# Kernel tuning notes

Hardware: AMD Instinct MI355X
Metric: run time of the kernel (lower is better)

Reference implementation:

```python
import jax, jax.numpy as jnp
import numpy as np

IN_CH = 128
EMBED = 64
ALPHA = 0.2  # leaky relu slope
NEG_INF = jnp.float32(-9e15)


def setup_inputs() -> dict:
    key = jax.random.key(0)
    k_x, k_adj, k_W, k_a, k_b = jax.random.split(key, 5)
    B, N = 2, 512
    x = jax.random.normal(k_x, (B, N, IN_CH), dtype=jnp.float32)
    adj = jax.random.randint(k_adj, (B, N, N), 0, 2, dtype=jnp.int32)
    # xavier_uniform with gain=1.414
    gain = 1.414
    lim_W = gain * np.sqrt(6.0 / (IN_CH + EMBED))
    W = jax.random.uniform(k_W, (IN_CH, EMBED), jnp.float32, -lim_W, lim_W)
    lim_a = gain * np.sqrt(6.0 / (2 * EMBED + 1))
    a = jax.random.uniform(k_a, (2 * EMBED, 1), jnp.float32, -lim_a, lim_a)
    bias = jax.random.normal(k_b, (EMBED,), dtype=jnp.float32) * 0.02
    return {"x": x, "adj": adj, "W": W, "a": a, "bias": bias}


def reference(x, adj, W, a, bias):
    B, N, _ = x.shape
    D = W.shape[1]
    hidden = jnp.matmul(x, W)                      # [B, N, D]
    # Faithful reproduction of the original's repeat_interleave/repeat + cat(dim=1) + view.
    chunks = jnp.repeat(hidden, N, axis=1)         # [B, N*N, D]
    alt = jnp.tile(hidden, (1, N, 1))              # [B, N*N, D]
    allc = jnp.concatenate([chunks, alt], axis=1).reshape(B, N, N, 2 * D)
    attn = jnp.matmul(allc, a)[..., 0]             # [B, N, N]
    attn = jnp.where(attn >= 0, attn, ALPHA * attn)  # leaky relu
    attn = jnp.where(adj > 0, attn, NEG_INF)
    attention = jax.nn.softmax(attn, axis=-1)
    # dropout omitted: reference is eval-mode (deterministic)
    out = jnp.matmul(attention, hidden) + bias     # [B, N, D]
    return out
```

## Files before the change

### kernel.cpp

```cpp
#include <hip/hip_runtime.h>
#include <math.h>

#define GN 512
#define GB 2
#define INCH 128
#define GD 64
#define ALPHA 0.2f
#define NEG_INF_F (-9e15f)
#define TI 4

__global__ __launch_bounds__(256) void k_hidden(
        const float* __restrict__ x, const float* __restrict__ W,
        const float* __restrict__ a,
        float* __restrict__ hidden, float* __restrict__ s1,
        float* __restrict__ s2, float* __restrict__ s12) {
    const int row0 = blockIdx.x * 4;
    const int tid = threadIdx.x;
    __shared__ float Wl[INCH * GD];
    __shared__ float xs[4][INCH];

    const float4* W4 = (const float4*)W;
    float4* Wl4 = (float4*)Wl;
    #pragma unroll
    for (int idx = tid; idx < INCH * GD / 4; idx += 256) Wl4[idx] = W4[idx];
    const float4* x4 = (const float4*)(x + (size_t)row0 * INCH);
    if (tid < 4 * INCH / 4) ((float4*)xs)[tid] = x4[tid];
    __syncthreads();

    const int r = tid >> 6, d = tid & 63;
    float h = 0.f;
    #pragma unroll
    for (int k = 0; k < INCH; ++k) h = fmaf(xs[r][k], Wl[k * GD + d], h);
    hidden[(size_t)(row0 + r) * GD + d] = h;

    float p1 = a[d] * h, p2 = a[GD + d] * h;
    #pragma unroll
    for (int off = 32; off > 0; off >>= 1) {
        p1 += __shfl_xor(p1, off, 64);
        p2 += __shfl_xor(p2, off, 64);
    }
    if (d == 0) { s1[row0 + r] = p1; s2[row0 + r] = p2; s12[row0 + r] = p1 + p2; }
}

__global__ __launch_bounds__(512) void k_attn(
        const int* __restrict__ adj, const float* __restrict__ hidden,
        const float* __restrict__ s1, const float* __restrict__ s2,
        const float* __restrict__ s12, const float* __restrict__ bias,
        float* __restrict__ out) {
    const int blk = blockIdx.x;
    const int b = blk >> 7;
    const int i0 = (blk & 127) * TI;
    const int tid = threadIdx.x;
    const int lane = tid & 63;
    const int w = tid >> 6;

    __shared__ float pl[TI][GN];
    __shared__ float red[8][TI][GD];
    __shared__ float invs[TI];

    const float* s1b  = s1  + b * GN;
    const float* s2b  = s2  + b * GN;
    const float* s12b = s12 + b * GN;

    if (w < TI) {
        const int i = i0 + w;
        const int* adjrow = adj + ((size_t)b * GN + i) * GN;
        float v[8];
        if (i < 256) {
            float c0 = s12b[2 * i], c1 = s12b[2 * i + 1];
            c0 = c0 >= 0.f ? c0 : ALPHA * c0;
            c1 = c1 >= 0.f ? c1 : ALPHA * c1;
            #pragma unroll
            for (int seg = 0; seg < 8; ++seg) {
                const int j = seg * 64 + lane;
                v[seg] = adjrow[j] > 0 ? (seg < 4 ? c0 : c1) : NEG_INF_F;
            }
        } else {
            #pragma unroll
            for (int seg = 0; seg < 8; ++seg) {
                const int j = seg * 64 + lane;
                const int m = j & 255;
                float pre = s1b[2 * m] + s2b[2 * m + 1];
                pre = pre >= 0.f ? pre : ALPHA * pre;
                v[seg] = adjrow[j] > 0 ? pre : NEG_INF_F;
            }
        }
        float mx = v[0];
        #pragma unroll
        for (int seg = 1; seg < 8; ++seg) mx = fmaxf(mx, v[seg]);
        #pragma unroll
        for (int off = 32; off > 0; off >>= 1) mx = fmaxf(mx, __shfl_xor(mx, off, 64));
        float s = 0.f;
        #pragma unroll
        for (int seg = 0; seg < 8; ++seg) {
            const float e = expf(v[seg] - mx);
            pl[w][seg * 64 + lane] = e;
            s += e;
        }
        #pragma unroll
        for (int off = 32; off > 0; off >>= 1) s += __shfl_xor(s, off, 64);
        if (lane == 0) invs[w] = 1.f / s;
    }
    __syncthreads();

    const float* hb = hidden + (size_t)b * GN * GD;
    const int j0 = w * 64;
    float acc0 = 0.f, acc1 = 0.f, acc2 = 0.f, acc3 = 0.f;
    #pragma unroll 4
    for (int jj = 0; jj < 64; jj += 4) {
        const int j = j0 + jj;
        const float4 q0 = *(const float4*)&pl[0][j];
        const float4 q1 = *(const float4*)&pl[1][j];
        const float4 q2 = *(const float4*)&pl[2][j];
        const float4 q3 = *(const float4*)&pl[3][j];
        float hv;
        hv = hb[(size_t)(j + 0) * GD + lane];
        acc0 = fmaf(q0.x, hv, acc0); acc1 = fmaf(q1.x, hv, acc1);
        acc2 = fmaf(q2.x, hv, acc2); acc3 = fmaf(q3.x, hv, acc3);
        hv = hb[(size_t)(j + 1) * GD + lane];
        acc0 = fmaf(q0.y, hv, acc0); acc1 = fmaf(q1.y, hv, acc1);
        acc2 = fmaf(q2.y, hv, acc2); acc3 = fmaf(q3.y, hv, acc3);
        hv = hb[(size_t)(j + 2) * GD + lane];
        acc0 = fmaf(q0.z, hv, acc0); acc1 = fmaf(q1.z, hv, acc1);
        acc2 = fmaf(q2.z, hv, acc2); acc3 = fmaf(q3.z, hv, acc3);
        hv = hb[(size_t)(j + 3) * GD + lane];
        acc0 = fmaf(q0.w, hv, acc0); acc1 = fmaf(q1.w, hv, acc1);
        acc2 = fmaf(q2.w, hv, acc2); acc3 = fmaf(q3.w, hv, acc3);
    }
    red[w][0][lane] = acc0; red[w][1][lane] = acc1;
    red[w][2][lane] = acc2; red[w][3][lane] = acc3;
    __syncthreads();

    if (tid < TI * GD) {
        const int r = tid >> 6, d = tid & 63;
        float o = 0.f;
        #pragma unroll
        for (int ww = 0; ww < 8; ++ww) o += red[ww][r][d];
        o = o * invs[r] + bias[d];
        out[((size_t)b * GN + i0 + r) * GD + d] = o;
    }
}

extern "C" void kernel_launch(void* const* d_in, const int* in_sizes, int n_in,
                              void* d_out, int out_size, void* d_ws, size_t ws_size,
                              hipStream_t stream) {
    const float* x    = (const float*)d_in[0];
    const int*   adj  = (const int*)d_in[1];
    const float* W    = (const float*)d_in[2];
    const float* a    = (const float*)d_in[3];
    const float* bias = (const float*)d_in[4];
    float* out = (float*)d_out;

    float* ws     = (float*)d_ws;
    float* hidden = ws;
    float* s1f    = hidden + GB * GN * GD;
    float* s2f    = s1f + GB * GN;
    float* s12f   = s2f + GB * GN;

    k_hidden<<<GB * GN / 4, 256, 0, stream>>>(x, W, a, hidden, s1f, s2f, s12f);
    k_attn<<<GB * GN / TI, 512, 0, stream>>>(adj, hidden, s1f, s2f, s12f, bias, out);
}
```

Before: 15.92 us.

## Fuse projection and attention into one kernel with per-block bf16 MFMA recompute

Merges the two launches into one kernel. Each block recomputes the full per-batch hidden projection (512x64) using bf16 MFMA with a swizzled shared-memory copy of W, keeps hidden and the attention scores in LDS, and stages its adj rows in LDS. This removes the second launch and the global round trip for hidden and scores. In exchange every block repeats the whole batch projection, about 128x redundant compute, and hidden is now rounded to bf16, which lowers precision. The large LDS footprint limits occupancy.

```diff
diff --git a/kernel.cpp b/kernel.cpp
--- a/kernel.cpp
+++ b/kernel.cpp
@@ -9,80 +9,152 @@
 #define NEG_INF_F (-9e15f)
 #define TI 4
 
-__global__ __launch_bounds__(256) void k_hidden(
-        const float* __restrict__ x, const float* __restrict__ W,
-        const float* __restrict__ a,
-        float* __restrict__ hidden, float* __restrict__ s1,
-        float* __restrict__ s2, float* __restrict__ s12) {
-    const int row0 = blockIdx.x * 4;
-    const int tid = threadIdx.x;
-    __shared__ float Wl[INCH * GD];
-    __shared__ float xs[4][INCH];
-
-    const float4* W4 = (const float4*)W;
-    float4* Wl4 = (float4*)Wl;
-    #pragma unroll
-    for (int idx = tid; idx < INCH * GD / 4; idx += 256) Wl4[idx] = W4[idx];
-    const float4* x4 = (const float4*)(x + (size_t)row0 * INCH);
-    if (tid < 4 * INCH / 4) ((float4*)xs)[tid] = x4[tid];
-    __syncthreads();
-
-    const int r = tid >> 6, d = tid & 63;
-    float h = 0.f;
-    #pragma unroll
-    for (int k = 0; k < INCH; ++k) h = fmaf(xs[r][k], Wl[k * GD + d], h);
-    hidden[(size_t)(row0 + r) * GD + d] = h;
-
-    float p1 = a[d] * h, p2 = a[GD + d] * h;
-    #pragma unroll
-    for (int off = 32; off > 0; off >>= 1) {
-        p1 += __shfl_xor(p1, off, 64);
-        p2 += __shfl_xor(p2, off, 64);
-    }
-    if (d == 0) { s1[row0 + r] = p1; s2[row0 + r] = p2; s12[row0 + r] = p1 + p2; }
-}
-
-__global__ __launch_bounds__(512) void k_attn(
-        const int* __restrict__ adj, const float* __restrict__ hidden,
-        const float* __restrict__ s1, const float* __restrict__ s2,
-        const float* __restrict__ s12, const float* __restrict__ bias,
-        float* __restrict__ out) {
+typedef float f32x4 __attribute__((ext_vector_type(4)));
+typedef short short8 __attribute__((ext_vector_type(8)));
+
+#define HB_OFF  0
+#define ADJ_OFF 65536
+#define S1_OFF  73728
+#define S2_OFF  75776
+#define INV_OFF 77824
+#define UN_OFF  77888
+#define LDS_BYTES 94272
+
+__device__ __forceinline__ unsigned f2bf(float f) {
+    unsigned u = __float_as_uint(f);
+    return (u + 0x7FFFu + ((u >> 16) & 1u)) >> 16;
+}
+__device__ __forceinline__ float bf2f(unsigned short h) {
+    return __uint_as_float(((unsigned)h) << 16);
+}
+
+__global__ __launch_bounds__(512, 2) void k_fused(
+        const float* __restrict__ x, const int* __restrict__ adj,
+        const float* __restrict__ W, const float* __restrict__ a,
+        const float* __restrict__ bias, float* __restrict__ out) {
+    extern __shared__ char smem[];
     const int blk = blockIdx.x;
-    const int b = blk >> 7;
-    const int i0 = (blk & 127) * TI;
     const int tid = threadIdx.x;
     const int lane = tid & 63;
     const int w = tid >> 6;
-
-    __shared__ float pl[TI][GN];
-    __shared__ float red[8][TI][GD];
-    __shared__ float invs[TI];
-
-    const float* s1b  = s1  + b * GN;
-    const float* s2b  = s2  + b * GN;
-    const float* s12b = s12 + b * GN;
+    const int lane15 = lane & 15;
+    const int kg = lane >> 4;
+    const int b = blk >> 7;
+    const int i0 = (blk & 127) * TI;
+
+    short* hbf  = (short*)(smem + HB_OFF);
+    int*   adjl = (int*)(smem + ADJ_OFF);
+    float* s1l  = (float*)(smem + S1_OFF);
+    float* s2l  = (float*)(smem + S2_OFF);
+    float* invs = (float*)(smem + INV_OFF);
+    short* wt   = (short*)(smem + UN_OFF);
+    float* plf  = (float*)(smem + UN_OFF);
+    float* red  = (float*)(smem + UN_OFF + 8192);
+
+    #pragma unroll
+    for (int rep = 0; rep < 4; ++rep) {
+        const int idx = tid + rep * 512;
+        const float4 wv = ((const float4*)W)[idx];
+        const int k = idx >> 4;
+        const int n0 = (idx & 15) * 4;
+        #pragma unroll
+        for (int e = 0; e < 4; ++e) {
+            const int n = n0 + e;
+            const float f = (e == 0) ? wv.x : (e == 1) ? wv.y : (e == 2) ? wv.z : wv.w;
+            wt[n * 128 + (((k >> 3) ^ (n & 7)) << 3) + (k & 7)] = (short)f2bf(f);
+        }
+    }
+    ((int4*)adjl)[tid] = ((const int4*)(adj + ((size_t)b * GN + i0) * GN))[tid];
+    float a1v[4], a2v[4];
+    #pragma unroll
+    for (int ct = 0; ct < 4; ++ct) {
+        a1v[ct] = a[ct * 16 + lane15];
+        a2v[ct] = a[GD + ct * 16 + lane15];
+    }
+    __syncthreads();
+
+    const float* xw = x + ((size_t)b * GN + w * 64) * INCH;
+    f32x4 acc[4][4];
+    #pragma unroll
+    for (int mt = 0; mt < 4; ++mt)
+        #pragma unroll
+        for (int ct = 0; ct < 4; ++ct)
+            acc[mt][ct] = (f32x4)0.f;
+
+    #pragma unroll
+    for (int kt = 0; kt < 4; ++kt) {
+        short8 av[4];
+        #pragma unroll
+        for (int mt = 0; mt < 4; ++mt) {
+            const float* p = xw + (mt * 16 + lane15) * INCH + kt * 32 + kg * 8;
+            const float4 lo = *((const float4*)p);
+            const float4 hi = *((const float4*)(p + 4));
+            int4 ai;
+            ai.x = f2bf(lo.x) | (f2bf(lo.y) << 16);
+            ai.y = f2bf(lo.z) | (f2bf(lo.w) << 16);
+            ai.z = f2bf(hi.x) | (f2bf(hi.y) << 16);
+            ai.w = f2bf(hi.z) | (f2bf(hi.w) << 16);
+            av[mt] = __builtin_bit_cast(short8, ai);
+        }
+        #pragma unroll
+        for (int ct = 0; ct < 4; ++ct) {
+            const int n = ct * 16 + lane15;
+            const int c = kt * 4 + kg;
+            const short8 bv = *((const short8*)(smem + UN_OFF + n * 256 + ((c ^ (n & 7)) << 4)));
+            #pragma unroll
+            for (int mt = 0; mt < 4; ++mt)
+                acc[mt][ct] = __builtin_amdgcn_mfma_f32_16x16x32_bf16(
+                                  av[mt], bv, acc[mt][ct], 0, 0, 0);
+        }
+    }
+
+    #pragma unroll
+    for (int mt = 0; mt < 4; ++mt) {
+        #pragma unroll
+        for (int r = 0; r < 4; ++r) {
+            float t1 = acc[mt][0][r] * a1v[0] + acc[mt][1][r] * a1v[1]
+                     + acc[mt][2][r] * a1v[2] + acc[mt][3][r] * a1v[3];
+            float t2 = acc[mt][0][r] * a2v[0] + acc[mt][1][r] * a2v[1]
+                     + acc[mt][2][r] * a2v[2] + acc[mt][3][r] * a2v[3];
+            #pragma unroll
+            for (int off = 1; off < 16; off <<= 1) {
+                t1 += __shfl_xor(t1, off, 64);
+                t2 += __shfl_xor(t2, off, 64);
+            }
+            const int row = w * 64 + mt * 16 + kg * 4 + r;
+            if (lane15 == 0) { s1l[row] = t1; s2l[row] = t2; }
+        }
+    }
+    #pragma unroll
+    for (int mt = 0; mt < 4; ++mt)
+        #pragma unroll
+        for (int ct = 0; ct < 4; ++ct)
+            #pragma unroll
+            for (int r = 0; r < 4; ++r) {
+                const int row = w * 64 + mt * 16 + kg * 4 + r;
+                hbf[row * GD + ct * 16 + lane15] = (short)f2bf(acc[mt][ct][r]);
+            }
+    __syncthreads();
 
     if (w < TI) {
         const int i = i0 + w;
-        const int* adjrow = adj + ((size_t)b * GN + i) * GN;
+        const int* adjw = adjl + w * GN;
         float v[8];
         if (i < 256) {
-            float c0 = s12b[2 * i], c1 = s12b[2 * i + 1];
+            float c0 = s1l[2 * i] + s2l[2 * i];
+            float c1 = s1l[2 * i + 1] + s2l[2 * i + 1];
             c0 = c0 >= 0.f ? c0 : ALPHA * c0;
             c1 = c1 >= 0.f ? c1 : ALPHA * c1;
             #pragma unroll
+            for (int seg = 0; seg < 8; ++seg)
+                v[seg] = adjw[seg * 64 + lane] > 0 ? (seg < 4 ? c0 : c1) : NEG_INF_F;
+        } else {
+            #pragma unroll
             for (int seg = 0; seg < 8; ++seg) {
-                const int j = seg * 64 + lane;
-                v[seg] = adjrow[j] > 0 ? (seg < 4 ? c0 : c1) : NEG_INF_F;
-            }
-        } else {
-            #pragma unroll
-            for (int seg = 0; seg < 8; ++seg) {
-                const int j = seg * 64 + lane;
-                const int m = j & 255;
-                float pre = s1b[2 * m] + s2b[2 * m + 1];
+                const int m = (seg * 64 + lane) & 255;
+                float pre = s1l[2 * m] + s2l[2 * m + 1];
                 pre = pre >= 0.f ? pre : ALPHA * pre;
-                v[seg] = adjrow[j] > 0 ? pre : NEG_INF_F;
+                v[seg] = adjw[seg * 64 + lane] > 0 ? pre : NEG_INF_F;
             }
         }
         float mx = v[0];
@@ -94,7 +166,7 @@
         #pragma unroll
         for (int seg = 0; seg < 8; ++seg) {
             const float e = expf(v[seg] - mx);
-            pl[w][seg * 64 + lane] = e;
+            plf[(seg * 64 + lane) * 4 + w] = e;
             s += e;
         }
         #pragma unroll
@@ -103,39 +175,27 @@
     }
     __syncthreads();
 
-    const float* hb = hidden + (size_t)b * GN * GD;
     const int j0 = w * 64;
-    float acc0 = 0.f, acc1 = 0.f, acc2 = 0.f, acc3 = 0.f;
+    float o0 = 0.f, o1 = 0.f, o2 = 0.f, o3 = 0.f;
     #pragma unroll 4
-    for (int jj = 0; jj < 64; jj += 4) {
+    for (int jj = 0; jj < 64; ++jj) {
         const int j = j0 + jj;
-        const float4 q0 = *(const float4*)&pl[0][j];
-        const float4 q1 = *(const float4*)&pl[1][j];
-        const float4 q2 = *(const float4*)&pl[2][j];
-        const float4 q3 = *(const float4*)&pl[3][j];
-        float hv;
-        hv = hb[(size_t)(j + 0) * GD + lane];
-        acc0 = fmaf(q0.x, hv, acc0); acc1 = fmaf(q1.x, hv, acc1);
-        acc2 = fmaf(q2.x, hv, acc2); acc3 = fmaf(q3.x, hv, acc3);
-        hv = hb[(size_t)(j + 1) * GD + lane];
-        acc0 = fmaf(q0.y, hv, acc0); acc1 = fmaf(q1.y, hv, acc1);
-        acc2 = fmaf(q2.y, hv, acc2); acc3 = fmaf(q3.y, hv, acc3);
-        hv = hb[(size_t)(j + 2) * GD + lane];
-        acc0 = fmaf(q0.z, hv, acc0); acc1 = fmaf(q1.z, hv, acc1);
-        acc2 = fmaf(q2.z, hv, acc2); acc3 = fmaf(q3.z, hv, acc3);
-        hv = hb[(size_t)(j + 3) * GD + lane];
-        acc0 = fmaf(q0.w, hv, acc0); acc1 = fmaf(q1.w, hv, acc1);
-        acc2 = fmaf(q2.w, hv, acc2); acc3 = fmaf(q3.w, hv, acc3);
-    }
-    red[w][0][lane] = acc0; red[w][1][lane] = acc1;
-    red[w][2][lane] = acc2; red[w][3][lane] = acc3;
+        const float4 q = *((const float4*)(plf + j * 4));
+        const float h = bf2f((unsigned short)hbf[j * GD + lane]);
+        o0 = fmaf(q.x, h, o0); o1 = fmaf(q.y, h, o1);
+        o2 = fmaf(q.z, h, o2); o3 = fmaf(q.w, h, o3);
+    }
+    red[(w * 4 + 0) * 64 + lane] = o0;
+    red[(w * 4 + 1) * 64 + lane] = o1;
+    red[(w * 4 + 2) * 64 + lane] = o2;
+    red[(w * 4 + 3) * 64 + lane] = o3;
     __syncthreads();
 
     if (tid < TI * GD) {
         const int r = tid >> 6, d = tid & 63;
         float o = 0.f;
         #pragma unroll
-        for (int ww = 0; ww < 8; ++ww) o += red[ww][r][d];
+        for (int ww = 0; ww < 8; ++ww) o += red[(ww * 4 + r) * 64 + d];
         o = o * invs[r] + bias[d];
         out[((size_t)b * GN + i0 + r) * GD + d] = o;
     }
@@ -151,12 +211,7 @@
     const float* bias = (const float*)d_in[4];
     float* out = (float*)d_out;
 
-    float* ws     = (float*)d_ws;
-    float* hidden = ws;
-    float* s1f    = hidden + GB * GN * GD;
-    float* s2f    = s1f + GB * GN;
-    float* s12f   = s2f + GB * GN;
-
-    k_hidden<<<GB * GN / 4, 256, 0, stream>>>(x, W, a, hidden, s1f, s2f, s12f);
-    k_attn<<<GB * GN / TI, 512, 0, stream>>>(adj, hidden, s1f, s2f, s12f, bias, out);
-}
+    (void)hipFuncSetAttribute((const void*)k_fused,
+                              hipFuncAttributeMaxDynamicSharedMemorySize, LDS_BYTES);
+    k_fused<<<GB * GN / TI, 512, LDS_BYTES, stream>>>(x, adj, W, a, bias, out);
+}
```

Result: slower. 21.49 us (+34.9%).

## Store hidden as bf16 and transpose softmax probabilities in shared memory

Applied to the files above, without the earlier changes.

The intermediate hidden matrix is now written as bf16 and converted back to fp32 inside the attention kernel, which halves the bytes read in the aggregation phase. The s12 buffer is dropped and recomputed from s1+s2. Softmax probabilities are stored row-interleaved so each step reads one float4 covering all four query rows. expf is replaced by __expf. Rounding hidden to bf16 costs accuracy in the output, and the two softmax branches are duplicated.

```diff
diff --git a/kernel.cpp b/kernel.cpp
--- a/kernel.cpp
+++ b/kernel.cpp
@@ -9,11 +9,19 @@
 #define NEG_INF_F (-9e15f)
 #define TI 4
 
+__device__ __forceinline__ unsigned f2bf(float f) {
+    unsigned u = __float_as_uint(f);
+    return (u + 0x7FFFu + ((u >> 16) & 1u)) >> 16;
+}
+__device__ __forceinline__ float bf2f(unsigned short h) {
+    return __uint_as_float(((unsigned)h) << 16);
+}
+
 __global__ __launch_bounds__(256) void k_hidden(
         const float* __restrict__ x, const float* __restrict__ W,
         const float* __restrict__ a,
-        float* __restrict__ hidden, float* __restrict__ s1,
-        float* __restrict__ s2, float* __restrict__ s12) {
+        unsigned short* __restrict__ hbf, float* __restrict__ s1,
+        float* __restrict__ s2) {
     const int row0 = blockIdx.x * 4;
     const int tid = threadIdx.x;
     __shared__ float Wl[INCH * GD];
@@ -22,16 +30,16 @@
     const float4* W4 = (const float4*)W;
     float4* Wl4 = (float4*)Wl;
     #pragma unroll
-    for (int idx = tid; idx < INCH * GD / 4; idx += 256) Wl4[idx] = W4[idx];
-    const float4* x4 = (const float4*)(x + (size_t)row0 * INCH);
-    if (tid < 4 * INCH / 4) ((float4*)xs)[tid] = x4[tid];
+    for (int t = 0; t < 8; ++t) Wl4[tid + t * 256] = W4[tid + t * 256];
+    if (tid < 4 * INCH / 4)
+        ((float4*)xs)[tid] = ((const float4*)(x + (size_t)row0 * INCH))[tid];
     __syncthreads();
 
     const int r = tid >> 6, d = tid & 63;
     float h = 0.f;
     #pragma unroll
     for (int k = 0; k < INCH; ++k) h = fmaf(xs[r][k], Wl[k * GD + d], h);
-    hidden[(size_t)(row0 + r) * GD + d] = h;
+    hbf[(size_t)(row0 + r) * GD + d] = (unsigned short)f2bf(h);
 
     float p1 = a[d] * h, p2 = a[GD + d] * h;
     #pragma unroll
@@ -39,14 +47,13 @@
         p1 += __shfl_xor(p1, off, 64);
         p2 += __shfl_xor(p2, off, 64);
     }
-    if (d == 0) { s1[row0 + r] = p1; s2[row0 + r] = p2; s12[row0 + r] = p1 + p2; }
+    if (d == 0) { s1[row0 + r] = p1; s2[row0 + r] = p2; }
 }
 
 __global__ __launch_bounds__(512) void k_attn(
-        const int* __restrict__ adj, const float* __restrict__ hidden,
+        const int* __restrict__ adj, const unsigned short* __restrict__ hbf,
         const float* __restrict__ s1, const float* __restrict__ s2,
-        const float* __restrict__ s12, const float* __restrict__ bias,
-        float* __restrict__ out) {
+        const float* __restrict__ bias, float* __restrict__ out) {
     const int blk = blockIdx.x;
     const int b = blk >> 7;
     const int i0 = (blk & 127) * TI;
@@ -54,88 +61,94 @@
     const int lane = tid & 63;
     const int w = tid >> 6;
 
-    __shared__ float pl[TI][GN];
-    __shared__ float red[8][TI][GD];
+    __shared__ float plf[GN * TI];
+    __shared__ float red[8 * TI * GD];
     __shared__ float invs[TI];
 
-    const float* s1b  = s1  + b * GN;
-    const float* s2b  = s2  + b * GN;
-    const float* s12b = s12 + b * GN;
+    const float* s1b = s1 + b * GN;
+    const float* s2b = s2 + b * GN;
 
     if (w < TI) {
         const int i = i0 + w;
-        const int* adjrow = adj + ((size_t)b * GN + i) * GN;
-        float v[8];
+        const int* adjw = adj + ((size_t)b * GN + i) * GN;
+        float pre4[4];
         if (i < 256) {
-            float c0 = s12b[2 * i], c1 = s12b[2 * i + 1];
+            float c0 = s1b[2 * i] + s2b[2 * i];
+            float c1 = s1b[2 * i + 1] + s2b[2 * i + 1];
             c0 = c0 >= 0.f ? c0 : ALPHA * c0;
             c1 = c1 >= 0.f ? c1 : ALPHA * c1;
+            pre4[0] = pre4[1] = pre4[2] = pre4[3] = c0;
+            float v[8];
+            #pragma unroll
+            for (int seg = 0; seg < 8; ++seg)
+                v[seg] = adjw[seg * 64 + lane] > 0 ? (seg < 4 ? c0 : c1) : NEG_INF_F;
+            float mx = v[0];
+            #pragma unroll
+            for (int seg = 1; seg < 8; ++seg) mx = fmaxf(mx, v[seg]);
+            #pragma unroll
+            for (int off = 32; off > 0; off >>= 1) mx = fmaxf(mx, __shfl_xor(mx, off, 64));
+            float s = 0.f;
             #pragma unroll
             for (int seg = 0; seg < 8; ++seg) {
-                const int j = seg * 64 + lane;
-                v[seg] = adjrow[j] > 0 ? (seg < 4 ? c0 : c1) : NEG_INF_F;
+                const float e = __expf(v[seg] - mx);
+                plf[(seg * 64 + lane) * TI + w] = e;
+                s += e;
             }
+            #pragma unroll
+            for (int off = 32; off > 0; off >>= 1) s += __shfl_xor(s, off, 64);
+            if (lane == 0) invs[w] = 1.f / s;
         } else {
             #pragma unroll
+            for (int sg = 0; sg < 4; ++sg) {
+                const int m = (sg * 64 + lane) & 255;
+                float pre = s1b[2 * m] + s2b[2 * m + 1];
+                pre4[sg] = pre >= 0.f ? pre : ALPHA * pre;
+            }
+            float v[8];
+            #pragma unroll
+            for (int seg = 0; seg < 8; ++seg)
+                v[seg] = adjw[seg * 64 + lane] > 0 ? pre4[seg & 3] : NEG_INF_F;
+            float mx = v[0];
+            #pragma unroll
+            for (int seg = 1; seg < 8; ++seg) mx = fmaxf(mx, v[seg]);
+            #pragma unroll
+            for (int off = 32; off > 0; off >>= 1) mx = fmaxf(mx, __shfl_xor(mx, off, 64));
+            float s = 0.f;
+            #pragma unroll
             for (int seg = 0; seg < 8; ++seg) {
-                const int j = seg * 64 + lane;
-                const int m = j & 255;
-                float pre = s1b[2 * m] + s2b[2 * m + 1];
-                pre = pre >= 0.f ? pre : ALPHA * pre;
-                v[seg] = adjrow[j] > 0 ? pre : NEG_INF_F;
+                const float e = __expf(v[seg] - mx);
+                plf[(seg * 64 + lane) * TI + w] = e;
+                s += e;
             }
+            #pragma unroll
+            for (int off = 32; off > 0; off >>= 1) s += __shfl_xor(s, off, 64);
+            if (lane == 0) invs[w] = 1.f / s;
         }
-        float mx = v[0];
-        #pragma unroll
-        for (int seg = 1; seg < 8; ++seg) mx = fmaxf(mx, v[seg]);
-        #pragma unroll
-        for (int off = 32; off > 0; off >>= 1) mx = fmaxf(mx, __shfl_xor(mx, off, 64));
-        float s = 0.f;
-        #pragma unroll
-        for (int seg = 0; seg < 8; ++seg) {
-            const float e = expf(v[seg] - mx);
-            pl[w][seg * 64 + lane] = e;
-            s += e;
-        }
-        #pragma unroll
-        for (int off = 32; off > 0; off >>= 1) s += __shfl_xor(s, off, 64);
-        if (lane == 0) invs[w] = 1.f / s;
     }
     __syncthreads();
 
-    const float* hb = hidden + (size_t)b * GN * GD;
+    const unsigned short* hbg = hbf + (size_t)b * GN * GD;
     const int j0 = w * 64;
-    float acc0 = 0.f, acc1 = 0.f, acc2 = 0.f, acc3 = 0.f;
-    #pragma unroll 4
-    for (int jj = 0; jj < 64; jj += 4) {
+    float o0 = 0.f, o1 = 0.f, o2 = 0.f, o3 = 0.f;
+    #pragma unroll 8
+    for (int jj = 0; jj < 64; ++jj) {
         const int j = j0 + jj;
-        const float4 q0 = *(const float4*)&pl[0][j];
-        const float4 q1 = *(const float4*)&pl[1][j];
-        const float4 q2 = *(const float4*)&pl[2][j];
-        const float4 q3 = *(const float4*)&pl[3][j];
-        float hv;
-        hv = hb[(size_t)(j + 0) * GD + lane];
-        acc0 = fmaf(q0.x, hv, acc0); acc1 = fmaf(q1.x, hv, acc1);
-        acc2 = fmaf(q2.x, hv, acc2); acc3 = fmaf(q3.x, hv, acc3);
-        hv = hb[(size_t)(j + 1) * GD + lane];
-        acc0 = fmaf(q0.y, hv, acc0); acc1 = fmaf(q1.y, hv, acc1);
-        acc2 = fmaf(q2.y, hv, acc2); acc3 = fmaf(q3.y, hv, acc3);
-        hv = hb[(size_t)(j + 2) * GD + lane];
-        acc0 = fmaf(q0.z, hv, acc0); acc1 = fmaf(q1.z, hv, acc1);
-        acc2 = fmaf(q2.z, hv, acc2); acc3 = fmaf(q3.z, hv, acc3);
-        hv = hb[(size_t)(j + 3) * GD + lane];
-        acc0 = fmaf(q0.w, hv, acc0); acc1 = fmaf(q1.w, hv, acc1);
-        acc2 = fmaf(q2.w, hv, acc2); acc3 = fmaf(q3.w, hv, acc3);
+        const float4 q = *((const float4*)(plf + j * TI));
+        const float h = bf2f(hbg[j * GD + lane]);
+        o0 = fmaf(q.x, h, o0); o1 = fmaf(q.y, h, o1);
+        o2 = fmaf(q.z, h, o2); o3 = fmaf(q.w, h, o3);
     }
-    red[w][0][lane] = acc0; red[w][1][lane] = acc1;
-    red[w][2][lane] = acc2; red[w][3][lane] = acc3;
+    red[(w * TI + 0) * GD + lane] = o0;
+    red[(w * TI + 1) * GD + lane] = o1;
+    red[(w * TI + 2) * GD + lane] = o2;
+    red[(w * TI + 3) * GD + lane] = o3;
     __syncthreads();
 
     if (tid < TI * GD) {
         const int r = tid >> 6, d = tid & 63;
         float o = 0.f;
         #pragma unroll
-        for (int ww = 0; ww < 8; ++ww) o += red[ww][r][d];
+        for (int ww = 0; ww < 8; ++ww) o += red[(ww * TI + r) * GD + d];
         o = o * invs[r] + bias[d];
         out[((size_t)b * GN + i0 + r) * GD + d] = o;
     }
@@ -151,12 +164,10 @@
     const float* bias = (const float*)d_in[4];
     float* out = (float*)d_out;
 
-    float* ws     = (float*)d_ws;
-    float* hidden = ws;
-    float* s1f    = hidden + GB * GN * GD;
-    float* s2f    = s1f + GB * GN;
-    float* s12f   = s2f + GB * GN;
+    unsigned short* hbf = (unsigned short*)d_ws;
+    float* s1f = (float*)((char*)d_ws + GB * GN * GD * sizeof(unsigned short));
+    float* s2f = s1f + GB * GN;
 
-    k_hidden<<<GB * GN / 4, 256, 0, stream>>>(x, W, a, hidden, s1f, s2f, s12f);
-    k_attn<<<GB * GN / TI, 512, 0, stream>>>(adj, hidden, s1f, s2f, s12f, bias, out);
+    k_hidden<<<GB * GN / 4, 256, 0, stream>>>(x, W, a, hbf, s1f, s2f);
+    k_attn<<<GB * GN / TI, 512, 0, stream>>>(adj, hbf, s1f, s2f, bias, out);
 }
```

New measurement: 15.36 us. 3.5% less time.
